# Kernel tuning notes

Hardware: AMD Instinct MI355X
Metric: run time of the kernel (lower is better)

The kernel has to match this reference:

```python
import jax, jax.numpy as jnp
import numpy as np

N, C, L = 128, 12, 2048
D = 8          # num_dilations: int(log2((L-1)/8)) + 1
DIV = 2        # divisor = min(2, g)
G = 64
H = G // DIV   # 32 groups
K = 8          # kernels per group
CP = 6         # num_channels_per = clip(C//2, 2, 8)
KW = 9         # kernel width


def setup_inputs() -> dict:
    key = jax.random.key(0)
    kx, kw, ki = jax.random.split(key, 3)
    X = jax.random.normal(kx, (N, C, L), dtype=jnp.float32)
    W = jax.random.normal(kw, (D, DIV, K * H, 1, KW), dtype=jnp.float32)
    W = W - W.mean(-1, keepdims=True)
    W = W / jnp.abs(W).sum(-1, keepdims=True)
    I = jax.random.randint(ki, (D, DIV, H, CP), 0, C).astype(jnp.int32)
    return {"X": X, "W": W, "I": I}


def _counts(Zc, n, h, k):
    # Zc: [n, h, k, Lout]. Reduce over k (kernel axis), histogram arg into k bins.
    Lout = Zc.shape[-1]
    max_vals = Zc.max(axis=2)                      # [n, h, Lout]
    max_idx = Zc.argmax(axis=2)                    # [n, h, Lout]
    min_idx = Zc.argmin(axis=2)                    # [n, h, Lout]
    base = (jnp.arange(n * h, dtype=jnp.int32) * k)[:, None]  # [n*h, 1]
    fmax = (base + max_idx.reshape(n * h, Lout)).reshape(-1)
    fmin = (base + min_idx.reshape(n * h, Lout)).reshape(-1)
    cmax = jnp.zeros(n * h * k, Zc.dtype).at[fmax].add(max_vals.reshape(-1)).reshape(n, h, k)
    cmin = jnp.zeros(n * h * k, Zc.dtype).at[fmin].add(jnp.asarray(1.0, Zc.dtype)).reshape(n, h, k)
    return cmax, cmin


def _forward(X, W, I):
    n = X.shape[0]
    diff_X = jnp.diff(X, axis=-1)  # [n, C, L-1]
    outs = []
    for di in range(D):
        d = 2 ** di
        p = (KW - 1) * d // 2
        for df in range(DIV):
            src = X if df == 0 else diff_X
            # channel gather + sum over selected channels: [n, H, Lsrc]
            inp = src[:, I[di, df]].sum(axis=2)
            # grouped dilated conv1d: groups=H, k outputs per group
            Zc = jax.lax.conv_general_dilated(
                inp, W[di, df],
                window_strides=(1,), padding=[(p, p)],
                rhs_dilation=(d,),
                dimension_numbers=("NCH", "OIH", "NCH"),
                feature_group_count=H,
            )  # [n, K*H, Lout]  (channel order is group-major: g*K + j)
            Zc = Zc.reshape(n, H, K, Zc.shape[-1])
            cmax, cmin = _counts(Zc, n, H, K)
            outs.append(cmax)
            outs.append(cmin)
    return jnp.concatenate(outs, axis=1).reshape(n, -1)  # [n, D*DIV*2*H*K]


def reference(X, W, I) -> jnp.ndarray:
    return _forward(X, W, I)
```

## Files before the change

### kernel.cpp

```cpp
#include <hip/hip_runtime.h>

#define N_   128
#define C_   12
#define L_   2048
#define H_   32
#define K_   8
#define CP_  6
#define KW_  9
#define FEAT_ 8192

template<int DIL, bool GUARD>
__device__ __forceinline__ void conv_phase(const float* __restrict__ s,
                                           const float* __restrict__ wr,
                                           float* __restrict__ cx,
                                           int* __restrict__ cn,
                                           const int lane)
{
    if constexpr (DIL == 1) {
        #pragma unroll 2
        for (int g = 0; g < 8; ++g) {
            const int t = g * 256 + 4 * lane;
            float win[12];
            #pragma unroll
            for (int q = 0; q < 3; ++q) {
                const float4 v = *(const float4*)(s + t + 4 * q);
                win[4*q+0] = v.x; win[4*q+1] = v.y;
                win[4*q+2] = v.z; win[4*q+3] = v.w;
            }
            #pragma unroll
            for (int p = 0; p < 4; ++p) {
                if (GUARD && g == 7 && p == 3 && lane == 63) continue;
                float a0 = 0.f, a1 = 0.f, a2 = 0.f, a3 = 0.f,
                      a4 = 0.f, a5 = 0.f, a6 = 0.f, a7 = 0.f;
                #pragma unroll
                for (int w = 0; w < KW_; ++w) {
                    const float v = win[p + w];
                    a0 = fmaf(v, wr[0 * KW_ + w], a0);
                    a1 = fmaf(v, wr[1 * KW_ + w], a1);
                    a2 = fmaf(v, wr[2 * KW_ + w], a2);
                    a3 = fmaf(v, wr[3 * KW_ + w], a3);
                    a4 = fmaf(v, wr[4 * KW_ + w], a4);
                    a5 = fmaf(v, wr[5 * KW_ + w], a5);
                    a6 = fmaf(v, wr[6 * KW_ + w], a6);
                    a7 = fmaf(v, wr[7 * KW_ + w], a7);
                }
                const float mxa = fmaxf(fmaxf(a0, a1), a2);
                const float mxb = fmaxf(fmaxf(a3, a4), a5);
                const float mxc = fmaxf(fmaxf(a6, a7), mxa);
                const float mx  = fmaxf(mxb, mxc);
                const float mna = fminf(fminf(a0, a1), a2);
                const float mnb = fminf(fminf(a3, a4), a5);
                const float mnc = fminf(fminf(a6, a7), mna);
                const float mn  = fminf(mnb, mnc);
                cx[0] += (a0 == mx) ? a0 : 0.f;  cn[0] += (a0 == mn);
                cx[1] += (a1 == mx) ? a1 : 0.f;  cn[1] += (a1 == mn);
                cx[2] += (a2 == mx) ? a2 : 0.f;  cn[2] += (a2 == mn);
                cx[3] += (a3 == mx) ? a3 : 0.f;  cn[3] += (a3 == mn);
                cx[4] += (a4 == mx) ? a4 : 0.f;  cn[4] += (a4 == mn);
                cx[5] += (a5 == mx) ? a5 : 0.f;  cn[5] += (a5 == mn);
                cx[6] += (a6 == mx) ? a6 : 0.f;  cn[6] += (a6 == mn);
                cx[7] += (a7 == mx) ? a7 : 0.f;  cn[7] += (a7 == mn);
            }
        }
    } else {
        #pragma unroll 4
        for (int g = 0; g < 16; ++g) {
            const int t = g * 128 + 2 * lane;
            float2 wv[9];
            #pragma unroll
            for (int w = 0; w < KW_; ++w)
                wv[w] = *(const float2*)(s + t + w * DIL);
            #pragma unroll
            for (int p = 0; p < 2; ++p) {
                if (GUARD && g == 15 && p == 1 && lane == 63) continue;
                float a0 = 0.f, a1 = 0.f, a2 = 0.f, a3 = 0.f,
                      a4 = 0.f, a5 = 0.f, a6 = 0.f, a7 = 0.f;
                #pragma unroll
                for (int w = 0; w < KW_; ++w) {
                    const float v = p ? wv[w].y : wv[w].x;
                    a0 = fmaf(v, wr[0 * KW_ + w], a0);
                    a1 = fmaf(v, wr[1 * KW_ + w], a1);
                    a2 = fmaf(v, wr[2 * KW_ + w], a2);
                    a3 = fmaf(v, wr[3 * KW_ + w], a3);
                    a4 = fmaf(v, wr[4 * KW_ + w], a4);
                    a5 = fmaf(v, wr[5 * KW_ + w], a5);
                    a6 = fmaf(v, wr[6 * KW_ + w], a6);
                    a7 = fmaf(v, wr[7 * KW_ + w], a7);
                }
                const float mxa = fmaxf(fmaxf(a0, a1), a2);
                const float mxb = fmaxf(fmaxf(a3, a4), a5);
                const float mxc = fmaxf(fmaxf(a6, a7), mxa);
                const float mx  = fmaxf(mxb, mxc);
                const float mna = fminf(fminf(a0, a1), a2);
                const float mnb = fminf(fminf(a3, a4), a5);
                const float mnc = fminf(fminf(a6, a7), mna);
                const float mn  = fminf(mnb, mnc);
                cx[0] += (a0 == mx) ? a0 : 0.f;  cn[0] += (a0 == mn);
                cx[1] += (a1 == mx) ? a1 : 0.f;  cn[1] += (a1 == mn);
                cx[2] += (a2 == mx) ? a2 : 0.f;  cn[2] += (a2 == mn);
                cx[3] += (a3 == mx) ? a3 : 0.f;  cn[3] += (a3 == mn);
                cx[4] += (a4 == mx) ? a4 : 0.f;  cn[4] += (a4 == mn);
                cx[5] += (a5 == mx) ? a5 : 0.f;  cn[5] += (a5 == mn);
                cx[6] += (a6 == mx) ? a6 : 0.f;  cn[6] += (a6 == mn);
                cx[7] += (a7 == mx) ? a7 : 0.f;  cn[7] += (a7 == mn);
            }
        }
    }
}

__global__ __launch_bounds__(64, 3) void hydra_kernel(
    const float* __restrict__ X,
    const float* __restrict__ W,
    const int*   __restrict__ I,
    float* __restrict__ out)
{
    __shared__ __align__(16) float s_conv[3072];

    const int lane  = threadIdx.x;
    const int b_raw = blockIdx.x;
    const int xcd   = b_raw & 7;
    const int sub   = b_raw >> 3;
    const int n     = xcd * 16 + (sub >> 9);
    const int rem   = sub & 511;
    const int comb  = rem & 15;
    const int h     = rem >> 4;

    const int df   = comb & 1;
    const int di   = comb >> 1;
    const int d    = 1 << di;
    const int Lsrc = L_ - df;
    const int pad  = 4 * d;

    for (int j = lane; j < pad; j += 64)               s_conv[j] = 0.0f;
    for (int j = pad + Lsrc + lane; j < 3072; j += 64) s_conv[j] = 0.0f;

    const int* Ib = I + (comb * H_ + h) * CP_;
    const int c0 = Ib[0], c1 = Ib[1], c2 = Ib[2],
              c3 = Ib[3], c4 = Ib[4], c5 = Ib[5];
    const float* Xn = X + (size_t)n * (C_ * L_);
    const float* xp0 = Xn + c0 * L_;
    const float* xp1 = Xn + c1 * L_;
    const float* xp2 = Xn + c2 * L_;
    const float* xp3 = Xn + c3 * L_;
    const float* xp4 = Xn + c4 * L_;
    const float* xp5 = Xn + c5 * L_;

    const float* Wb = W + (size_t)(comb * (K_ * H_) + h * K_) * KW_;
    float wr[K_ * KW_];
    #pragma unroll
    for (int q = 0; q < K_ * KW_; ++q) wr[q] = Wb[q];

    #pragma unroll
    for (int c = 0; c < 4; ++c) {
        float sl[8];
        {
            float l0[8], l1[8], l2[8];
            #pragma unroll
            for (int j = 0; j < 8; ++j) {
                const int t = c * 512 + lane + j * 64;
                l0[j] = xp0[t]; l1[j] = xp1[t]; l2[j] = xp2[t];
            }
            #pragma unroll
            for (int j = 0; j < 8; ++j) sl[j] = (l0[j] + l1[j]) + l2[j];
        }
        {
            float l0[8], l1[8], l2[8];
            #pragma unroll
            for (int j = 0; j < 8; ++j) {
                const int t = c * 512 + lane + j * 64;
                l0[j] = xp3[t]; l1[j] = xp4[t]; l2[j] = xp5[t];
            }
            #pragma unroll
            for (int j = 0; j < 8; ++j) sl[j] += (l0[j] + l1[j]) + l2[j];
        }
        #pragma unroll
        for (int j = 0; j < 8; ++j)
            s_conv[pad + c * 512 + lane + j * 64] = sl[j];
    }

    if (df == 1) {
        float dv[32];
        #pragma unroll
        for (int c = 0; c < 4; ++c)
            #pragma unroll
            for (int j = 0; j < 8; ++j) {
                const int t = c * 512 + lane + j * 64;
                dv[c * 8 + j] = s_conv[pad + t + 1] - s_conv[pad + t];
            }
        #pragma unroll
        for (int c = 0; c < 4; ++c)
            #pragma unroll
            for (int j = 0; j < 8; ++j) {
                const int t = c * 512 + lane + j * 64;
                s_conv[pad + t] = (t == 2047) ? 0.0f : dv[c * 8 + j];
            }
    }

    float cx[K_] = {0.f, 0.f, 0.f, 0.f, 0.f, 0.f, 0.f, 0.f};
    int   cn[K_] = {0, 0, 0, 0, 0, 0, 0, 0};

    switch (comb) {
        case  0: conv_phase<  1, false>(s_conv, wr, cx, cn, lane); break;
        case  1: conv_phase<  1, true >(s_conv, wr, cx, cn, lane); break;
        case  2: conv_phase<  2, false>(s_conv, wr, cx, cn, lane); break;
        case  3: conv_phase<  2, true >(s_conv, wr, cx, cn, lane); break;
        case  4: conv_phase<  4, false>(s_conv, wr, cx, cn, lane); break;
        case  5: conv_phase<  4, true >(s_conv, wr, cx, cn, lane); break;
        case  6: conv_phase<  8, false>(s_conv, wr, cx, cn, lane); break;
        case  7: conv_phase<  8, true >(s_conv, wr, cx, cn, lane); break;
        case  8: conv_phase< 16, false>(s_conv, wr, cx, cn, lane); break;
        case  9: conv_phase< 16, true >(s_conv, wr, cx, cn, lane); break;
        case 10: conv_phase< 32, false>(s_conv, wr, cx, cn, lane); break;
        case 11: conv_phase< 32, true >(s_conv, wr, cx, cn, lane); break;
        case 12: conv_phase< 64, false>(s_conv, wr, cx, cn, lane); break;
        case 13: conv_phase< 64, true >(s_conv, wr, cx, cn, lane); break;
        case 14: conv_phase<128, false>(s_conv, wr, cx, cn, lane); break;
        default: conv_phase<128, true >(s_conv, wr, cx, cn, lane); break;
    }

    float red[16];
    #pragma unroll
    for (int k = 0; k < K_; ++k) { red[k] = cx[k]; red[8 + k] = (float)cn[k]; }
    #pragma unroll
    for (int off = 1; off < 64; off <<= 1) {
        #pragma unroll
        for (int q = 0; q < 16; ++q)
            red[q] += __shfl_xor(red[q], off, 64);
    }
    if (lane == 0) {
        float* ob = out + (size_t)n * FEAT_ + (comb * 2) * (H_ * K_) + h * K_;
        #pragma unroll
        for (int k = 0; k < K_; ++k) ob[k] = red[k];
        #pragma unroll
        for (int k = 0; k < K_; ++k) ob[H_ * K_ + k] = red[8 + k];
    }
}

extern "C" void kernel_launch(void* const* d_in, const int* in_sizes, int n_in,
                              void* d_out, int out_size, void* d_ws, size_t ws_size,
                              hipStream_t stream) {
    const float* X = (const float*)d_in[0];
    const float* W = (const float*)d_in[1];
    const int*   I = (const int*)d_in[2];
    float* out = (float*)d_out;

    const int blocks = N_ * 16 * H_;
    hipLaunchKernelGGL(hydra_kernel, dim3(blocks), dim3(64), 0, stream,
                       X, W, I, out);
}
```

Baseline: 385.9 us.

## Split each block's sequence across two wavefronts with shared-memory reduction

Each block now runs 128 threads (two wavefronts), and each wave loads, sums and convolves half of the 2048-sample sequence. The two partial max/min counts are combined through a small shared array after a barrier. The diff step now works in registers using shuffles plus one extra global load per wave at the halo, replacing the read-back from shared memory. The goal is more parallelism per block and less serial work per wave, at the cost of block-level syncs and launch bounds that limit registers more tightly.

New measurement: 413.4 us. 1.07x slower.

```diff
diff --git a/kernel.cpp b/kernel.cpp
--- a/kernel.cpp
+++ b/kernel.cpp
@@ -14,11 +14,12 @@
                                            const float* __restrict__ wr,
                                            float* __restrict__ cx,
                                            int* __restrict__ cn,
-                                           const int lane)
+                                           const int lane, const int wid)
 {
     if constexpr (DIL == 1) {
-        #pragma unroll 2
-        for (int g = 0; g < 8; ++g) {
+        #pragma unroll
+        for (int gg = 0; gg < 4; ++gg) {
+            const int g = wid * 4 + gg;
             const int t = g * 256 + 4 * lane;
             float win[12];
             #pragma unroll
@@ -64,7 +65,8 @@
         }
     } else {
         #pragma unroll 4
-        for (int g = 0; g < 16; ++g) {
+        for (int gg = 0; gg < 8; ++gg) {
+            const int g = wid * 8 + gg;
             const int t = g * 128 + 2 * lane;
             float2 wv[9];
             #pragma unroll
@@ -108,15 +110,18 @@
     }
 }
 
-__global__ __launch_bounds__(64, 3) void hydra_kernel(
+__global__ __launch_bounds__(128, 4) void hydra_kernel(
     const float* __restrict__ X,
     const float* __restrict__ W,
     const int*   __restrict__ I,
     float* __restrict__ out)
 {
     __shared__ __align__(16) float s_conv[3072];
-
-    const int lane  = threadIdx.x;
+    __shared__ float s_red[32];
+
+    const int wid  = threadIdx.x >> 6;
+    const int lane = threadIdx.x & 63;
+
     const int b_raw = blockIdx.x;
     const int xcd   = b_raw & 7;
     const int sub   = b_raw >> 3;
@@ -131,8 +136,8 @@
     const int Lsrc = L_ - df;
     const int pad  = 4 * d;
 
-    for (int j = lane; j < pad; j += 64)               s_conv[j] = 0.0f;
-    for (int j = pad + Lsrc + lane; j < 3072; j += 64) s_conv[j] = 0.0f;
+    for (int j = threadIdx.x; j < pad; j += 128)               s_conv[j] = 0.0f;
+    for (int j = pad + Lsrc + threadIdx.x; j < 3072; j += 128) s_conv[j] = 0.0f;
 
     const int* Ib = I + (comb * H_ + h) * CP_;
     const int c0 = Ib[0], c1 = Ib[1], c2 = Ib[2],
@@ -150,72 +155,63 @@
     #pragma unroll
     for (int q = 0; q < K_ * KW_; ++q) wr[q] = Wb[q];
 
+    const int base = 1024 * wid;
+    float sl[16];
     #pragma unroll
     for (int c = 0; c < 4; ++c) {
-        float sl[8];
-        {
-            float l0[8], l1[8], l2[8];
-            #pragma unroll
-            for (int j = 0; j < 8; ++j) {
-                const int t = c * 512 + lane + j * 64;
-                l0[j] = xp0[t]; l1[j] = xp1[t]; l2[j] = xp2[t];
-            }
-            #pragma unroll
-            for (int j = 0; j < 8; ++j) sl[j] = (l0[j] + l1[j]) + l2[j];
-        }
-        {
-            float l0[8], l1[8], l2[8];
-            #pragma unroll
-            for (int j = 0; j < 8; ++j) {
-                const int t = c * 512 + lane + j * 64;
-                l0[j] = xp3[t]; l1[j] = xp4[t]; l2[j] = xp5[t];
-            }
-            #pragma unroll
-            for (int j = 0; j < 8; ++j) sl[j] += (l0[j] + l1[j]) + l2[j];
-        }
-        #pragma unroll
-        for (int j = 0; j < 8; ++j)
-            s_conv[pad + c * 512 + lane + j * 64] = sl[j];
-    }
-
-    if (df == 1) {
-        float dv[32];
-        #pragma unroll
-        for (int c = 0; c < 4; ++c)
-            #pragma unroll
-            for (int j = 0; j < 8; ++j) {
-                const int t = c * 512 + lane + j * 64;
-                dv[c * 8 + j] = s_conv[pad + t + 1] - s_conv[pad + t];
-            }
-        #pragma unroll
-        for (int c = 0; c < 4; ++c)
-            #pragma unroll
-            for (int j = 0; j < 8; ++j) {
-                const int t = c * 512 + lane + j * 64;
-                s_conv[pad + t] = (t == 2047) ? 0.0f : dv[c * 8 + j];
-            }
-    }
+        float l0[4], l1[4], l2[4], l3[4], l4[4], l5[4];
+        #pragma unroll
+        for (int j = 0; j < 4; ++j) {
+            const int t = base + c * 256 + j * 64 + lane;
+            l0[j] = xp0[t]; l1[j] = xp1[t]; l2[j] = xp2[t];
+            l3[j] = xp3[t]; l4[j] = xp4[t]; l5[j] = xp5[t];
+        }
+        #pragma unroll
+        for (int j = 0; j < 4; ++j)
+            sl[c * 4 + j] = ((l0[j] + l1[j]) + (l2[j] + l3[j])) + (l4[j] + l5[j]);
+    }
+
+    if (df == 0) {
+        #pragma unroll
+        for (int jj = 0; jj < 16; ++jj)
+            s_conv[pad + base + jj * 64 + lane] = sl[jj];
+    } else {
+        const int tx  = base + 1024;
+        const int txc = (tx < 2048) ? tx : 2047;
+        const float sx = ((xp0[txc] + xp1[txc]) + (xp2[txc] + xp3[txc]))
+                       + (xp4[txc] + xp5[txc]);
+        #pragma unroll
+        for (int jj = 0; jj < 16; ++jj) {
+            const float rot = __shfl_down(sl[jj], 1, 64);
+            const float bc  = (jj < 15) ? __shfl(sl[jj + 1], 0, 64) : sx;
+            const float nxt = (lane == 63) ? bc : rot;
+            const int t = base + jj * 64 + lane;
+            s_conv[pad + t] = (t == 2047) ? 0.0f : (nxt - sl[jj]);
+        }
+    }
+
+    __syncthreads();
 
     float cx[K_] = {0.f, 0.f, 0.f, 0.f, 0.f, 0.f, 0.f, 0.f};
     int   cn[K_] = {0, 0, 0, 0, 0, 0, 0, 0};
 
     switch (comb) {
-        case  0: conv_phase<  1, false>(s_conv, wr, cx, cn, lane); break;
-        case  1: conv_phase<  1, true >(s_conv, wr, cx, cn, lane); break;
-        case  2: conv_phase<  2, false>(s_conv, wr, cx, cn, lane); break;
-        case  3: conv_phase<  2, true >(s_conv, wr, cx, cn, lane); break;
-        case  4: conv_phase<  4, false>(s_conv, wr, cx, cn, lane); break;
-        case  5: conv_phase<  4, true >(s_conv, wr, cx, cn, lane); break;
-        case  6: conv_phase<  8, false>(s_conv, wr, cx, cn, lane); break;
-        case  7: conv_phase<  8, true >(s_conv, wr, cx, cn, lane); break;
-        case  8: conv_phase< 16, false>(s_conv, wr, cx, cn, lane); break;
-        case  9: conv_phase< 16, true >(s_conv, wr, cx, cn, lane); break;
-        case 10: conv_phase< 32, false>(s_conv, wr, cx, cn, lane); break;
-        case 11: conv_phase< 32, true >(s_conv, wr, cx, cn, lane); break;
-        case 12: conv_phase< 64, false>(s_conv, wr, cx, cn, lane); break;
-        case 13: conv_phase< 64, true >(s_conv, wr, cx, cn, lane); break;
-        case 14: conv_phase<128, false>(s_conv, wr, cx, cn, lane); break;
-        default: conv_phase<128, true >(s_conv, wr, cx, cn, lane); break;
+        case  0: conv_phase<  1, false>(s_conv, wr, cx, cn, lane, wid); break;
+        case  1: conv_phase<  1, true >(s_conv, wr, cx, cn, lane, wid); break;
+        case  2: conv_phase<  2, false>(s_conv, wr, cx, cn, lane, wid); break;
+        case  3: conv_phase<  2, true >(s_conv, wr, cx, cn, lane, wid); break;
+        case  4: conv_phase<  4, false>(s_conv, wr, cx, cn, lane, wid); break;
+        case  5: conv_phase<  4, true >(s_conv, wr, cx, cn, lane, wid); break;
+        case  6: conv_phase<  8, false>(s_conv, wr, cx, cn, lane, wid); break;
+        case  7: conv_phase<  8, true >(s_conv, wr, cx, cn, lane, wid); break;
+        case  8: conv_phase< 16, false>(s_conv, wr, cx, cn, lane, wid); break;
+        case  9: conv_phase< 16, true >(s_conv, wr, cx, cn, lane, wid); break;
+        case 10: conv_phase< 32, false>(s_conv, wr, cx, cn, lane, wid); break;
+        case 11: conv_phase< 32, true >(s_conv, wr, cx, cn, lane, wid); break;
+        case 12: conv_phase< 64, false>(s_conv, wr, cx, cn, lane, wid); break;
+        case 13: conv_phase< 64, true >(s_conv, wr, cx, cn, lane, wid); break;
+        case 14: conv_phase<128, false>(s_conv, wr, cx, cn, lane, wid); break;
+        default: conv_phase<128, true >(s_conv, wr, cx, cn, lane, wid); break;
     }
 
     float red[16];
@@ -228,11 +224,16 @@
             red[q] += __shfl_xor(red[q], off, 64);
     }
     if (lane == 0) {
-        float* ob = out + (size_t)n * FEAT_ + (comb * 2) * (H_ * K_) + h * K_;
-        #pragma unroll
-        for (int k = 0; k < K_; ++k) ob[k] = red[k];
-        #pragma unroll
-        for (int k = 0; k < K_; ++k) ob[H_ * K_ + k] = red[8 + k];
+        #pragma unroll
+        for (int q = 0; q < 16; ++q) s_red[wid * 16 + q] = red[q];
+    }
+    __syncthreads();
+
+    if (threadIdx.x < 16) {
+        const int s = threadIdx.x >> 3;
+        const int k = threadIdx.x & 7;
+        out[(size_t)n * FEAT_ + (comb * 2 + s) * (H_ * K_) + h * K_ + k] =
+            s_red[threadIdx.x] + s_red[16 + threadIdx.x];
     }
 }
 
@@ -245,6 +246,6 @@
     float* out = (float*)d_out;
 
     const int blocks = N_ * 16 * H_;
-    hipLaunchKernelGGL(hydra_kernel, dim3(blocks), dim3(64), 0, stream,
+    hipLaunchKernelGGL(hydra_kernel, dim3(blocks), dim3(128), 0, stream,
                        X, W, I, out);
 }
```
